# Kernel optimization log

Measured on AMD Instinct MI355X. Metric: run time of the kernel, lower is better.

The kernel has to match this reference:

```python
import jax, jax.numpy as jnp
import numpy as np
from jax import lax

B, T, V, L = 256, 512, 256, 64
EPS = 1e-7  # keras backend epsilon used by ctc_batch_cost
NEG = -1e30  # log(0) surrogate, safe in float32


def setup_inputs() -> dict:
    key = jax.random.key(0)
    k1, k2 = jax.random.split(key)
    # labels in [0, V-1): class V-1 is reserved for the CTC blank
    y_true = jax.random.randint(k1, (B, L), 0, V - 1)
    # ctc_batch_cost expects probabilities (softmax output)
    logits = jax.random.normal(k2, (B, T, V), dtype=jnp.float32)
    y_pred = jax.nn.softmax(logits, axis=-1)
    return {"y_true": y_true, "y_pred": y_pred}


def reference(y_true, y_pred):
    """Keras ctc_batch_cost: per-example CTC negative log-likelihood, shape [B,1].

    Matches TF semantics: blank = V-1, log(y_pred + eps), full input/label lengths,
    merge-repeated forward DP in log space.
    """
    b, t, v = y_pred.shape
    l = y_true.shape[1]
    S = 2 * l + 1  # extended label: blank-interleaved
    blank = v - 1

    logp = jnp.log(y_pred + EPS)  # [B,T,V]

    # extended label sequence z: blank at even positions, labels at odd
    ext = jnp.full((b, S), blank, dtype=y_true.dtype).at[:, 1::2].set(y_true)  # [B,S]

    # lp[b,t,s] = logp[b,t,ext[b,s]]
    idx = jnp.broadcast_to(ext[:, None, :], (b, t, S))
    lp = jnp.take_along_axis(logp, idx, axis=2)  # [B,T,S]

    # skip transition s-2 -> s allowed iff z[s] != blank and z[s] != z[s-2]
    ext_m2 = jnp.concatenate([jnp.full((b, 2), -1, dtype=ext.dtype), ext[:, :-2]], axis=1)
    skip = (ext != blank) & (ext != ext_m2)  # [B,S]

    # alpha at t=0: only first blank or first label reachable
    alpha0 = jnp.full((b, S), NEG, dtype=logp.dtype)
    alpha0 = alpha0.at[:, 0].set(lp[:, 0, 0]).at[:, 1].set(lp[:, 0, 1])

    neg1 = jnp.full((b, 1), NEG, dtype=logp.dtype)
    neg2 = jnp.full((b, 2), NEG, dtype=logp.dtype)

    def step(alpha, lpt):
        a1 = jnp.concatenate([neg1, alpha[:, :-1]], axis=1)
        a2 = jnp.concatenate([neg2, alpha[:, :-2]], axis=1)
        m = jnp.logaddexp(alpha, a1)
        m = jnp.where(skip, jnp.logaddexp(m, a2), m)
        return m + lpt, None

    lp_t = jnp.moveaxis(lp[:, 1:], 1, 0)  # [T-1, B, S] time-major
    alphaT, _ = lax.scan(step, alpha0, lp_t)

    loss = -jnp.logaddexp(alphaT[:, -1], alphaT[:, -2])  # [B]
    return loss[:, None]
```

## Files before the change

### kernel.cpp

```cpp
#include <hip/hip_runtime.h>
#include <math.h>


#define BB   256
#define TI   512
#define VV   256
#define LL   64
#define CH   32
#define NCH  (TI / CH)
#define RING 4
#define EPSF 1e-7f
#define LN2F 0.6931471805599453f

#if __has_builtin(__builtin_amdgcn_logf)
__device__ __forceinline__ float flog2(float x) { return __builtin_amdgcn_logf(x); }
#else
__device__ __forceinline__ float flog2(float x) { return __log2f(x); }
#endif

template <int CTRL>
__device__ __forceinline__ float dppf(float oldv, float v) {
    return __int_as_float(__builtin_amdgcn_update_dpp(
        __float_as_int(oldv), __float_as_int(v), CTRL, 0xF, 0xF, false));
}
__device__ __forceinline__ float shup0(float x) { return dppf<0x138>(0.0f, x); }

struct DP {
    float a0, a1, a128;
    float C;
    float f, fs;
    float skipf;
    int   lane;
};

__device__ __forceinline__ void rescale(DP& d) {
    float m  = fmaxf(fmaxf(d.a0, d.a1), d.a128);
    int   mi    = __float_as_int(m);
    int   ebits = mi & 0x7f800000;
    bool  dead  = (ebits == 0);
    float s = __int_as_float((254 << 23) - ebits);
    s = dead ? 1.0f : s;
    d.a0 *= s; d.a1 *= s; d.a128 *= s;
    float Ei  = (float)((mi >> 23) - 127);
    float Cm1 = shup0(d.C);
    d.C = dead ? Cm1 : (d.C + Ei);
    float Cm1b = shup0(d.C);
    int dCi = (int)(Cm1b - d.C);
    int e = dCi + 127;
    e = e < 0 ? 0 : (e > 254 ? 254 : e);
    float fn = __int_as_float(e << 23);
    d.f  = (d.lane == 0) ? 0.0f : fn;
    d.fs = d.f * d.skipf;
}

__device__ __forceinline__ void dp_step(DP& d, float pb, float pl) {
    float pa1 = shup0(d.a1);
    float s01 = d.a0 + d.a1;
    float na0   = fmaf(pa1, d.f,  d.a0) * pb;
    float na1   = fmaf(pa1, d.fs, s01)  * pl;
    float na128 = (d.a128 + d.a1) * pb;
    d.a0 = na0; d.a1 = na1; d.a128 = na128;
}

template <bool PA, bool FIRST>
__device__ __forceinline__ void dp_chunk(DP& d, const float (&pb)[CH],
                                         const float (&pl)[CH]) {
    #pragma unroll
    for (int tt = 0; tt < CH; ++tt) {
        if (FIRST && tt == 0) {
            d.a0 = (d.lane == 0) ? pb[0] : 0.0f;
            d.a1 = (d.lane == 0) ? pl[0] : 0.0f;
        } else {
            dp_step(d, pb[tt], pl[tt]);
        }
        if (PA || (tt & 7) == 7) rescale(d);
    }
}

__device__ __forceinline__ void stage_chunk(const float* __restrict__ src,
                                            int cc, int lane,
                                            float* __restrict__ lslot) {
    const float* g = src + (size_t)cc * CH * VV + lane * 4;
    #pragma unroll
    for (int r = 0; r < CH; ++r) {
        __builtin_amdgcn_global_load_lds(
            (const __attribute__((address_space(1))) void*)(g + r * VV),
            (__attribute__((address_space(3))) void*)(lslot + r * VV),
            16, 0, 0);
    }
}

__global__ __launch_bounds__(128) void ctc_kernel(
        const int* __restrict__ y_true,
        const float* __restrict__ y_pred,
        float* __restrict__ out) {
    __shared__ float ring[RING][CH * VV];

    const int b    = blockIdx.x;
    const int tid  = threadIdx.x;
    const int lane = tid & 63;
    const int wave = tid >> 6;
    const float* src = y_pred + (size_t)b * TI * VV;

    const int lab = y_true[b * LL + lane];

    DP d;
    d.lane = lane;
    {
        const int prevLab = __shfl_up(lab, 1);
        d.skipf = (lane == 0 || lab != prevLab) ? 1.0f : 0.0f;
    }
    d.a0 = 0.0f; d.a1 = 0.0f; d.a128 = 0.0f;
    d.C = 0.0f; d.f = 0.0f; d.fs = 0.0f;

    if (wave == 1) {
        stage_chunk(src, 0, lane, ring[0]);
        stage_chunk(src, 1, lane, ring[1]);
    }
    __syncthreads();

    for (int c = 0; c < NCH; ++c) {
        if (wave == 1) {
            if (c + 2 < NCH)
                stage_chunk(src, c + 2, lane, ring[(c + 2) & (RING - 1)]);
        } else {
            const float* base = ring[c & (RING - 1)];
            float pb[CH], pl[CH];
            #pragma unroll
            for (int i = 0; i < CH; ++i) {
                pb[i] = base[i * VV + (VV - 1)] + EPSF;
                pl[i] = base[i * VV + lab]      + EPSF;
            }
            if (c == 0)      dp_chunk<true,  true >(d, pb, pl);
            else if (c < 4)  dp_chunk<true,  false>(d, pb, pl);
            else             dp_chunk<false, false>(d, pb, pl);
        }
        __syncthreads();
    }

    if (wave == 0 && lane == 63) {
        float tail = fmaxf(d.a128 + d.a1, 1e-37f);
        out[b] = -LN2F * (d.C + flog2(tail));
    }
}

extern "C" void kernel_launch(void* const* d_in, const int* in_sizes, int n_in,
                              void* d_out, int out_size, void* d_ws, size_t ws_size,
                              hipStream_t stream) {
    const int*   y_true = (const int*)d_in[0];
    const float* y_pred = (const float*)d_in[1];
    float*       out    = (float*)d_out;
    ctc_kernel<<<dim3(BB), dim3(128), 0, stream>>>(y_true, y_pred, out);
}
```

Before: 196.0 us.

## Replace per-chunk block barriers with LDS flag producer-consumer pipeline

Replaces the __syncthreads after every chunk with a producer/consumer protocol built on two shared-memory counters. The loader wave streams chunks into an 8-slot ring, signalling completion through vmcnt waits. The DP wave spins on the producer count and releases slots once its LDS reads finish. Chunk size is halved and the ring doubled so the loader can run further ahead, removing the lockstep stalls between the two waves. The spin loops, manual waitcnt fences and volatile LDS flags add correctness risk around memory ordering.

```diff
diff --git a/kernel.cpp b/kernel.cpp
--- a/kernel.cpp
+++ b/kernel.cpp
@@ -6,11 +6,13 @@
 #define TI   512
 #define VV   256
 #define LL   64
-#define CH   32
+#define CH   16
 #define NCH  (TI / CH)
-#define RING 4
+#define RING 8
 #define EPSF 1e-7f
 #define LN2F 0.6931471805599453f
+
+#define CFENCE() asm volatile("" ::: "memory")
 
 #if __has_builtin(__builtin_amdgcn_logf)
 __device__ __forceinline__ float flog2(float x) { return __builtin_amdgcn_logf(x); }
@@ -78,14 +80,14 @@
 }
 
 __device__ __forceinline__ void stage_chunk(const float* __restrict__ src,
-                                            int cc, int lane,
-                                            float* __restrict__ lslot) {
-    const float* g = src + (size_t)cc * CH * VV + lane * 4;
+                                            int n, int lane,
+                                            float* __restrict__ slot) {
+    const float* g = src + (size_t)n * CH * VV + lane * 4;
     #pragma unroll
     for (int r = 0; r < CH; ++r) {
         __builtin_amdgcn_global_load_lds(
             (const __attribute__((address_space(1))) void*)(g + r * VV),
-            (__attribute__((address_space(3))) void*)(lslot + r * VV),
+            (__attribute__((address_space(3))) void*)(slot + r * VV),
             16, 0, 0);
     }
 }
@@ -95,6 +97,7 @@
         const float* __restrict__ y_pred,
         float* __restrict__ out) {
     __shared__ float ring[RING][CH * VV];
+    __shared__ int   prod_cnt, cons_cnt;
 
     const int b    = blockIdx.x;
     const int tid  = threadIdx.x;
@@ -102,28 +105,43 @@
     const int wave = tid >> 6;
     const float* src = y_pred + (size_t)b * TI * VV;
 
+    volatile int* vp = &prod_cnt;
+    volatile int* vc = &cons_cnt;
+
     const int lab = y_true[b * LL + lane];
 
-    DP d;
-    d.lane = lane;
-    {
-        const int prevLab = __shfl_up(lab, 1);
-        d.skipf = (lane == 0 || lab != prevLab) ? 1.0f : 0.0f;
-    }
-    d.a0 = 0.0f; d.a1 = 0.0f; d.a128 = 0.0f;
-    d.C = 0.0f; d.f = 0.0f; d.fs = 0.0f;
+    if (tid == 0) { prod_cnt = 0; cons_cnt = 0; }
+    __syncthreads();
 
     if (wave == 1) {
-        stage_chunk(src, 0, lane, ring[0]);
-        stage_chunk(src, 1, lane, ring[1]);
-    }
-    __syncthreads();
+        for (int n = 0; n < NCH; ++n) {
+            if (n >= RING) {
+                while (*vc < n - (RING - 1)) { }
+                CFENCE();
+            }
+            stage_chunk(src, n, lane, ring[n & (RING - 1)]);
+            if (n >= 2) {
+                asm volatile("s_waitcnt vmcnt(32)" ::: "memory");
+                if (lane == 0) *vp = n - 1;
+            }
+        }
+        asm volatile("s_waitcnt vmcnt(16)" ::: "memory");
+        if (lane == 0) *vp = NCH - 1;
+        asm volatile("s_waitcnt vmcnt(0)" ::: "memory");
+        if (lane == 0) *vp = NCH;
+    } else {
+        DP d;
+        d.lane = lane;
+        {
+            const int prevLab = __shfl_up(lab, 1);
+            d.skipf = (lane == 0 || lab != prevLab) ? 1.0f : 0.0f;
+        }
+        d.a0 = 0.0f; d.a1 = 0.0f; d.a128 = 0.0f;
+        d.C = 0.0f; d.f = 0.0f; d.fs = 0.0f;
 
-    for (int c = 0; c < NCH; ++c) {
-        if (wave == 1) {
-            if (c + 2 < NCH)
-                stage_chunk(src, c + 2, lane, ring[(c + 2) & (RING - 1)]);
-        } else {
+        for (int c = 0; c < NCH; ++c) {
+            while (*vp < c + 1) { }
+            CFENCE();
             const float* base = ring[c & (RING - 1)];
             float pb[CH], pl[CH];
             #pragma unroll
@@ -131,16 +149,18 @@
                 pb[i] = base[i * VV + (VV - 1)] + EPSF;
                 pl[i] = base[i * VV + lab]      + EPSF;
             }
+            asm volatile("s_waitcnt lgkmcnt(0)" ::: "memory");
+            if (lane == 0) *vc = c + 1;
+            CFENCE();
             if (c == 0)      dp_chunk<true,  true >(d, pb, pl);
-            else if (c < 4)  dp_chunk<true,  false>(d, pb, pl);
+            else if (c < 8)  dp_chunk<true,  false>(d, pb, pl);
             else             dp_chunk<false, false>(d, pb, pl);
         }
-        __syncthreads();
-    }
 
-    if (wave == 0 && lane == 63) {
-        float tail = fmaxf(d.a128 + d.a1, 1e-37f);
-        out[b] = -LN2F * (d.C + flog2(tail));
+        if (lane == 63) {
+            float tail = fmaxf(d.a128 + d.a1, 1e-37f);
+            out[b] = -LN2F * (d.C + flog2(tail));
+        }
     }
 }
 
```

Result: no change. 194.0 us (-1.0%).
